# Optimization experiments

Measured on AMD Instinct MI355X. Metric: run time of the kernel, lower is better.

## Reference

```python
import jax, jax.numpy as jnp
import numpy as np

BSZ, L, D_Q, S_Q = 2, 2048, 512, 4
EPS = 1e-6


def quat_mul(a, b):
    ar, ai, aj, ak = a[..., 0], a[..., 1], a[..., 2], a[..., 3]
    br, bi, bj, bk = b[..., 0], b[..., 1], b[..., 2], b[..., 3]
    return jnp.stack((
        ar * br - ai * bi - aj * bj - ak * bk,
        ar * bi + ai * br + aj * bk - ak * bj,
        ar * bj - ai * bk + aj * br + ak * bi,
        ar * bk + ai * bj - aj * bi + ak * br,
    ), axis=-1)


def quat_inv(q):
    r, i, j, k = q[..., 0], q[..., 1], q[..., 2], q[..., 3]
    s = 1.0 / (r * r + i * i + j * j + k * k + EPS)
    return jnp.stack((r * s, -i * s, -j * s, -k * s), axis=-1)


def setup_inputs() -> dict:
    key = jax.random.key(0)
    ks = jax.random.split(key, 8)
    u = jax.random.normal(ks[0], (BSZ, L, D_Q, 4), dtype=jnp.float32)
    dt = jax.random.uniform(ks[1], (BSZ, L, D_Q), dtype=jnp.float32)
    B_in = jax.random.normal(ks[2], (BSZ, L, S_Q, 4), dtype=jnp.float32)
    C_in = jax.random.normal(ks[3], (BSZ, L, S_Q, 4), dtype=jnp.float32)
    # A_log init: log(arange(1, S_q+1)) repeated over D_q rows
    A_log = jnp.tile(jnp.log(jnp.arange(1, S_Q + 1, dtype=jnp.float32)), (D_Q, 1))
    A_i = jax.random.normal(ks[4], (D_Q, S_Q), dtype=jnp.float32) * 0.01
    A_j = jax.random.normal(ks[5], (D_Q, S_Q), dtype=jnp.float32) * 0.01
    A_k = jax.random.normal(ks[6], (D_Q, S_Q), dtype=jnp.float32) * 0.01
    return {"u": u, "dt": dt, "B_in": B_in, "C_in": C_in,
            "A_log": A_log, "A_i": A_i, "A_j": A_j, "A_k": A_k}


def reference(u, dt, B_in, C_in, A_log, A_i, A_j, A_k):
    # A quaternion: real part -exp(A_log), imaginary parts A_i/j/k  [D_q, S_q, 4]
    A_quat = jnp.stack([-jnp.exp(A_log), A_i, A_j, A_k], axis=-1)
    dt_b = dt[..., None, None]                      # [B, L, D_q, 1, 1]
    z = dt_b * A_quat                               # [B, L, D_q, S_q, 4]
    one = jnp.zeros_like(z).at[..., 0].set(1.0)     # quaternion identity
    num = one + 0.5 * z
    den = one - 0.5 * z
    den_inv = quat_inv(den)
    q = quat_mul(den_inv, num)                      # Cayley transition [B,L,D_q,S_q,4]
    dB = quat_mul(den_inv * dt_b, B_in[:, :, None])  # [B,L,D_q,S_q,4]
    Bu = quat_mul(dB, u[:, :, :, None])             # [B,L,D_q,S_q,4]

    def step(h, qb):
        qt, but = qb
        h = quat_mul(qt, h) + but
        return h, h

    h0 = jnp.zeros((u.shape[0], u.shape[2], A_quat.shape[1], 4), u.dtype)
    _, h_all = jax.lax.scan(step, h0, (jnp.swapaxes(q, 0, 1), jnp.swapaxes(Bu, 0, 1)))
    h_all = jnp.swapaxes(h_all, 0, 1)               # [B, L, D_q, S_q, 4]
    yh = quat_mul(C_in[:, :, None], h_all)
    return yh.sum(axis=3)                           # [B, L, D_q, 4]
```

## Files before the change

kernel.cpp:

```cpp
#include <hip/hip_runtime.h>

#define BSZ   2
#define LSEQ  2048
#define DQ    512
#define SQ    4
#define EPSQ  1e-6f

typedef float nfloat4 __attribute__((ext_vector_type(4)));

struct Quat { float r, i, j, k; };

__device__ __forceinline__ Quat qmul(const Quat a, const Quat b) {
    Quat o;
    o.r = a.r*b.r - a.i*b.i - a.j*b.j - a.k*b.k;
    o.i = a.r*b.i + a.i*b.r + a.j*b.k - a.k*b.j;
    o.j = a.r*b.j - a.i*b.k + a.j*b.r + a.k*b.i;
    o.k = a.r*b.k + a.i*b.j - a.j*b.i + a.k*b.r;
    return o;
}

__device__ __forceinline__ Quat qmuladd(const Quat a, const Quat b, const Quat c) {
    Quat o;
    o.r = c.r + a.r*b.r - a.i*b.i - a.j*b.j - a.k*b.k;
    o.i = c.i + a.r*b.i + a.i*b.r + a.j*b.k - a.k*b.j;
    o.j = c.j + a.r*b.j - a.i*b.k + a.j*b.r + a.k*b.i;
    o.k = c.k + a.r*b.k + a.i*b.j - a.j*b.i + a.k*b.r;
    return o;
}

__device__ __forceinline__ Quat q_of(const float4 v) { return Quat{v.x, v.y, v.z, v.w}; }
__device__ __forceinline__ float4 f4_of(const Quat q) { return make_float4(q.r, q.i, q.j, q.k); }

__device__ __forceinline__ void cayley_step(const float a, const float4 hA,
                                            const float4 Bq, const float4 uq,
                                            Quat& q, Quat& Bu) {
    const float wr = a * hA.x;
    const float wi = a * hA.y;
    const float wj = a * hA.z;
    const float wk = a * hA.w;
    const float m  = wi*wi + wj*wj + wk*wk;
    const float e  = 1.0f - wr;
    const float dd = e*e + m + EPSQ;
    const float sv = __builtin_amdgcn_rcpf(dd);
    const float s2 = sv + sv;
    q.r = sv * (1.0f - (wr*wr + m));
    q.i = s2 * wi; q.j = s2 * wj; q.k = s2 * wk;
    const Quat cd{e, wi, wj, wk};
    const Quat cb = qmul(cd, q_of(Bq));
    const float as = a * sv;
    const Quat dB{as*cb.r, as*cb.i, as*cb.j, as*cb.k};
    Bu = qmul(dB, q_of(uq));
}

__device__ __forceinline__ float4 load_hA(const float* __restrict__ Alog,
                                          const float* __restrict__ Ai,
                                          const float* __restrict__ Aj,
                                          const float* __restrict__ Ak, int idx) {
    float4 hA;
    hA.x = -0.5f * expf(Alog[idx]);
    hA.y =  0.5f * Ai[idx];
    hA.z =  0.5f * Aj[idx];
    hA.w =  0.5f * Ak[idx];
    return hA;
}

template<int NCH>
__global__ __launch_bounds__(256) void qssm_pass1(
    const float* __restrict__ u, const float* __restrict__ dt,
    const float* __restrict__ Bin,
    const float* __restrict__ Alog, const float* __restrict__ Ai,
    const float* __restrict__ Aj,   const float* __restrict__ Ak,
    float4* __restrict__ WQ, float4* __restrict__ WB)
{
    constexpr int CH = LSEQ / NCH;
    const int d = blockIdx.x * 256 + threadIdx.x;
    const int c = blockIdx.y;
    const int b = blockIdx.z;
    const int t0 = c * CH;

    float4 hA[SQ];
#pragma unroll
    for (int s = 0; s < SQ; ++s) hA[s] = load_hA(Alog, Ai, Aj, Ak, d*SQ + s);

    const float*  dtp = dt + ((size_t)(b*LSEQ + t0))*DQ + d;
    const float4* up  = (const float4*)u   + ((size_t)(b*LSEQ + t0))*DQ + d;
    const float4* Bp  = (const float4*)Bin + ((size_t)(b*LSEQ + t0))*SQ;

    Quat Q[SQ], Bc[SQ];
    {
        const float  a  = dtp[0];
        const float4 uq = up[0];
#pragma unroll
        for (int s = 0; s < SQ; ++s) {
            Quat q, Bu;
            cayley_step(a, hA[s], Bp[s], uq, q, Bu);
            Q[s] = q; Bc[s] = Bu;
        }
    }
#pragma unroll
    for (int j = 1; j < CH; ++j) {
        const float  a  = dtp[(size_t)j*DQ];
        const float4 uq = up[(size_t)j*DQ];
#pragma unroll
        for (int s = 0; s < SQ; ++s) {
            Quat q, Bu;
            cayley_step(a, hA[s], Bp[j*SQ + s], uq, q, Bu);
            Bc[s] = qmuladd(q, Bc[s], Bu);
            Q[s]  = qmul(q, Q[s]);
        }
    }
#pragma unroll
    for (int s = 0; s < SQ; ++s) {
        const size_t idx = ((size_t)(b*SQ + s)*NCH + c)*DQ + d;
        WQ[idx] = f4_of(Q[s]);
        WB[idx] = f4_of(Bc[s]);
    }
}

template<int NCH>
__global__ __launch_bounds__(256) void qssm_pass2(
    const float4* __restrict__ WQ, float4* __restrict__ WB)
{
    constexpr int GS = 16;
    constexpr int NG = NCH / GS;
    __shared__ float4 QL[NG][16];
    __shared__ float4 BL[NG][16];
    __shared__ float4 HS[NG][16];

    const int t  = threadIdx.x;
    const int i  = t & 15;
    const int g  = t >> 4;
    const int bs = blockIdx.x >> 5;
    const int d  = (blockIdx.x & 31) * 16 + i;
    const size_t chbase = (size_t)bs * NCH * DQ + d;

    size_t idx = chbase + (size_t)(g * GS) * DQ;
    Quat Qa = q_of(WQ[idx]);
    Quat Ba = q_of(WB[idx]);
#pragma unroll
    for (int j = 1; j < GS; ++j) {
        idx += DQ;
        const Quat Qc = q_of(WQ[idx]);
        const Quat Bc = q_of(WB[idx]);
        Ba = qmuladd(Qc, Ba, Bc);
        Qa = qmul(Qc, Qa);
    }
    QL[g][i] = f4_of(Qa);
    BL[g][i] = f4_of(Ba);
    __syncthreads();

    if (t < 16) {
        Quat h{0.f, 0.f, 0.f, 0.f};
#pragma unroll
        for (int gg = 0; gg < NG; ++gg) {
            HS[gg][t] = f4_of(h);
            h = qmuladd(q_of(QL[gg][t]), h, q_of(BL[gg][t]));
        }
    }
    __syncthreads();

    Quat h = q_of(HS[g][i]);
    idx = chbase + (size_t)(g * GS) * DQ;
#pragma unroll
    for (int j = 0; j < GS; ++j) {
        const Quat Qc = q_of(WQ[idx]);
        const Quat Bc = q_of(WB[idx]);
        WB[idx] = f4_of(h);
        h = qmuladd(Qc, h, Bc);
        idx += DQ;
    }
}

template<int NCH>
__global__ __launch_bounds__(256) void qssm_pass3(
    const float* __restrict__ u, const float* __restrict__ dt,
    const float* __restrict__ Bin, const float* __restrict__ Cin,
    const float* __restrict__ Alog, const float* __restrict__ Ai,
    const float* __restrict__ Aj,   const float* __restrict__ Ak,
    const float4* __restrict__ WB, float* __restrict__ out)
{
    constexpr int CH = LSEQ / NCH;
    const int d = blockIdx.x * 256 + threadIdx.x;
    const int c = blockIdx.y;
    const int b = blockIdx.z;
    const int t0 = c * CH;

    float4 hA[SQ];
    Quat   h[SQ];
#pragma unroll
    for (int s = 0; s < SQ; ++s) {
        hA[s] = load_hA(Alog, Ai, Aj, Ak, d*SQ + s);
        h[s] = q_of(WB[((size_t)(b*SQ + s)*NCH + c)*DQ + d]);
    }
    const float*  dtp  = dt + ((size_t)(b*LSEQ + t0))*DQ + d;
    const float4* up   = (const float4*)u   + ((size_t)(b*LSEQ + t0))*DQ + d;
    const float4* Bp   = (const float4*)Bin + ((size_t)(b*LSEQ + t0))*SQ;
    const float4* Cp   = (const float4*)Cin + ((size_t)(b*LSEQ + t0))*SQ;
    nfloat4*      outp = (nfloat4*)out + ((size_t)(b*LSEQ + t0))*DQ + d;

#pragma unroll
    for (int j = 0; j < CH; ++j) {
        const float  a  = dtp[(size_t)j*DQ];
        const float4 uq = up[(size_t)j*DQ];
        Quat y{0.f, 0.f, 0.f, 0.f};
#pragma unroll
        for (int s = 0; s < SQ; ++s) {
            const float4 Cq = Cp[j*SQ + s];
            Quat q, Bu;
            cayley_step(a, hA[s], Bp[j*SQ + s], uq, q, Bu);
            h[s] = qmuladd(q, h[s], Bu);
            y = qmuladd(q_of(Cq), h[s], y);
        }
        const nfloat4 yv = {y.r, y.i, y.j, y.k};
        __builtin_nontemporal_store(yv, &outp[(size_t)j*DQ]);
    }
}

template<int NCH>
static void launch_all(const float* u, const float* dt, const float* Bin,
                       const float* Cin, const float* Alog, const float* Ai,
                       const float* Aj, const float* Ak,
                       float* out, void* d_ws, hipStream_t stream) {
    const size_t elems = (size_t)BSZ * SQ * NCH * DQ;
    float4* WQ = (float4*)d_ws;
    float4* WB = WQ + elems;
    dim3 g(DQ / 256, NCH, BSZ);
    qssm_pass1<NCH><<<g, 256, 0, stream>>>(u, dt, Bin, Alog, Ai, Aj, Ak, WQ, WB);
    qssm_pass2<NCH><<<(BSZ*SQ*DQ)/16, 16*(NCH/16), 0, stream>>>(WQ, WB);
    qssm_pass3<NCH><<<g, 256, 0, stream>>>(u, dt, Bin, Cin, Alog, Ai, Aj, Ak, WB, out);
}

extern "C" void kernel_launch(void* const* d_in, const int* in_sizes, int n_in,
                              void* d_out, int out_size, void* d_ws, size_t ws_size,
                              hipStream_t stream) {
    const float* u    = (const float*)d_in[0];
    const float* dt   = (const float*)d_in[1];
    const float* Bin  = (const float*)d_in[2];
    const float* Cin  = (const float*)d_in[3];
    const float* Alog = (const float*)d_in[4];
    const float* Ai   = (const float*)d_in[5];
    const float* Aj   = (const float*)d_in[6];
    const float* Ak   = (const float*)d_in[7];
    float* out = (float*)d_out;

    auto ws_need = [](int nch) -> size_t {
        return 2ull * BSZ * SQ * (size_t)nch * DQ * sizeof(float4);
    };
    if (ws_size >= ws_need(256)) {
        launch_all<256>(u, dt, Bin, Cin, Alog, Ai, Aj, Ak, out, d_ws, stream);
    } else if (ws_size >= ws_need(128)) {
        launch_all<128>(u, dt, Bin, Cin, Alog, Ai, Aj, Ak, out, d_ws, stream);
    } else {
        launch_all<64>(u, dt, Bin, Cin, Alog, Ai, Aj, Ak, out, d_ws, stream);
    }
}
```

Measured before the change: 164.8 us.

## Split state dimension across threads in scan passes to raise parallelism

Pass 1 now launches twice as many blocks, each thread handling two of the four state quaternions instead of all four. Pass 3 assigns the two state halves to the upper and lower 32 lanes of each wavefront and combines the partial outputs with a cross-lane shuffle before the store. Loop unrolling drops from full to 2 and pointer increments replace indexed addressing, with __expf replacing expf. This is meant to cut per-thread register pressure and add occupancy and parallelism, at the cost of loading u and dt redundantly per state half and the extra shuffle work.

```diff
diff --git a/kernel.cpp b/kernel.cpp
--- a/kernel.cpp
+++ b/kernel.cpp
@@ -57,7 +57,7 @@
                                           const float* __restrict__ Aj,
                                           const float* __restrict__ Ak, int idx) {
     float4 hA;
-    hA.x = -0.5f * expf(Alog[idx]);
+    hA.x = -0.5f * __expf(Alog[idx]);
     hA.y =  0.5f * Ai[idx];
     hA.z =  0.5f * Aj[idx];
     hA.w =  0.5f * Ak[idx];
@@ -73,47 +73,51 @@
     float4* __restrict__ WQ, float4* __restrict__ WB)
 {
     constexpr int CH = LSEQ / NCH;
-    const int d = blockIdx.x * 256 + threadIdx.x;
-    const int c = blockIdx.y;
-    const int b = blockIdx.z;
+    const int d  = blockIdx.x * 256 + threadIdx.x;
+    const int c  = blockIdx.y;
+    const int b  = blockIdx.z >> 1;
+    const int s0 = (blockIdx.z & 1) * 2;
     const int t0 = c * CH;
 
-    float4 hA[SQ];
-#pragma unroll
-    for (int s = 0; s < SQ; ++s) hA[s] = load_hA(Alog, Ai, Aj, Ak, d*SQ + s);
-
-    const float*  dtp = dt + ((size_t)(b*LSEQ + t0))*DQ + d;
-    const float4* up  = (const float4*)u   + ((size_t)(b*LSEQ + t0))*DQ + d;
-    const float4* Bp  = (const float4*)Bin + ((size_t)(b*LSEQ + t0))*SQ;
-
-    Quat Q[SQ], Bc[SQ];
+    float4 hA[2];
+    hA[0] = load_hA(Alog, Ai, Aj, Ak, d*SQ + s0);
+    hA[1] = load_hA(Alog, Ai, Aj, Ak, d*SQ + s0 + 1);
+
+    const int base = (b*LSEQ + t0);
+    const float*  dtp = dt + (size_t)base*DQ + d;
+    const float4* up  = (const float4*)u   + (size_t)base*DQ + d;
+    const float4* Bp  = (const float4*)Bin + (size_t)base*SQ + s0;
+
+    Quat Q[2], Bc[2];
     {
-        const float  a  = dtp[0];
-        const float4 uq = up[0];
-#pragma unroll
-        for (int s = 0; s < SQ; ++s) {
+        const float  a  = *dtp;
+        const float4 uq = *up;
+#pragma unroll
+        for (int ss = 0; ss < 2; ++ss) {
             Quat q, Bu;
-            cayley_step(a, hA[s], Bp[s], uq, q, Bu);
-            Q[s] = q; Bc[s] = Bu;
-        }
-    }
-#pragma unroll
+            cayley_step(a, hA[ss], Bp[ss], uq, q, Bu);
+            Q[ss] = q; Bc[ss] = Bu;
+        }
+        dtp += DQ; up += DQ; Bp += SQ;
+    }
+#pragma unroll 2
     for (int j = 1; j < CH; ++j) {
-        const float  a  = dtp[(size_t)j*DQ];
-        const float4 uq = up[(size_t)j*DQ];
-#pragma unroll
-        for (int s = 0; s < SQ; ++s) {
+        const float  a  = *dtp;
+        const float4 uq = *up;
+#pragma unroll
+        for (int ss = 0; ss < 2; ++ss) {
             Quat q, Bu;
-            cayley_step(a, hA[s], Bp[j*SQ + s], uq, q, Bu);
-            Bc[s] = qmuladd(q, Bc[s], Bu);
-            Q[s]  = qmul(q, Q[s]);
-        }
-    }
-#pragma unroll
-    for (int s = 0; s < SQ; ++s) {
-        const size_t idx = ((size_t)(b*SQ + s)*NCH + c)*DQ + d;
-        WQ[idx] = f4_of(Q[s]);
-        WB[idx] = f4_of(Bc[s]);
+            cayley_step(a, hA[ss], Bp[ss], uq, q, Bu);
+            Bc[ss] = qmuladd(q, Bc[ss], Bu);
+            Q[ss]  = qmul(q, Q[ss]);
+        }
+        dtp += DQ; up += DQ; Bp += SQ;
+    }
+#pragma unroll
+    for (int ss = 0; ss < 2; ++ss) {
+        const size_t idx = ((size_t)(b*SQ + s0 + ss)*NCH + c)*DQ + d;
+        WQ[idx] = f4_of(Q[ss]);
+        WB[idx] = f4_of(Bc[ss]);
     }
 }
 
@@ -180,39 +184,53 @@
     const float4* __restrict__ WB, float* __restrict__ out)
 {
     constexpr int CH = LSEQ / NCH;
-    const int d = blockIdx.x * 256 + threadIdx.x;
+    const int t    = threadIdx.x;
+    const int lane = t & 63;
+    const int wv   = t >> 6;
+    const int dl   = lane & 31;
+    const int sh   = lane >> 5;
+    const int s0   = sh * 2;
+    const int d = blockIdx.x * 128 + wv * 32 + dl;
     const int c = blockIdx.y;
     const int b = blockIdx.z;
     const int t0 = c * CH;
 
-    float4 hA[SQ];
-    Quat   h[SQ];
-#pragma unroll
-    for (int s = 0; s < SQ; ++s) {
-        hA[s] = load_hA(Alog, Ai, Aj, Ak, d*SQ + s);
-        h[s] = q_of(WB[((size_t)(b*SQ + s)*NCH + c)*DQ + d]);
-    }
-    const float*  dtp  = dt + ((size_t)(b*LSEQ + t0))*DQ + d;
-    const float4* up   = (const float4*)u   + ((size_t)(b*LSEQ + t0))*DQ + d;
-    const float4* Bp   = (const float4*)Bin + ((size_t)(b*LSEQ + t0))*SQ;
-    const float4* Cp   = (const float4*)Cin + ((size_t)(b*LSEQ + t0))*SQ;
-    nfloat4*      outp = (nfloat4*)out + ((size_t)(b*LSEQ + t0))*DQ + d;
-
-#pragma unroll
+    float4 hA[2];
+    Quat   h[2];
+#pragma unroll
+    for (int ss = 0; ss < 2; ++ss) {
+        hA[ss] = load_hA(Alog, Ai, Aj, Ak, d*SQ + s0 + ss);
+        h[ss] = q_of(WB[((size_t)(b*SQ + s0 + ss)*NCH + c)*DQ + d]);
+    }
+    const int base = (b*LSEQ + t0);
+    const float*  dtp  = dt + (size_t)base*DQ + d;
+    const float4* up   = (const float4*)u   + (size_t)base*DQ + d;
+    const float4* Bp   = (const float4*)Bin + (size_t)base*SQ + s0;
+    const float4* Cp   = (const float4*)Cin + (size_t)base*SQ + s0;
+    nfloat4*      outp = (nfloat4*)out + (size_t)base*DQ + d;
+
+#pragma unroll 2
     for (int j = 0; j < CH; ++j) {
-        const float  a  = dtp[(size_t)j*DQ];
-        const float4 uq = up[(size_t)j*DQ];
+        const float  a  = *dtp;
+        const float4 uq = *up;
         Quat y{0.f, 0.f, 0.f, 0.f};
 #pragma unroll
-        for (int s = 0; s < SQ; ++s) {
-            const float4 Cq = Cp[j*SQ + s];
+        for (int ss = 0; ss < 2; ++ss) {
+            const float4 Cq = Cp[ss];
             Quat q, Bu;
-            cayley_step(a, hA[s], Bp[j*SQ + s], uq, q, Bu);
-            h[s] = qmuladd(q, h[s], Bu);
-            y = qmuladd(q_of(Cq), h[s], y);
-        }
-        const nfloat4 yv = {y.r, y.i, y.j, y.k};
-        __builtin_nontemporal_store(yv, &outp[(size_t)j*DQ]);
+            cayley_step(a, hA[ss], Bp[ss], uq, q, Bu);
+            h[ss] = qmuladd(q, h[ss], Bu);
+            y = qmuladd(q_of(Cq), h[ss], y);
+        }
+        y.r += __shfl_xor(y.r, 32);
+        y.i += __shfl_xor(y.i, 32);
+        y.j += __shfl_xor(y.j, 32);
+        y.k += __shfl_xor(y.k, 32);
+        if (sh == 0) {
+            const nfloat4 yv = {y.r, y.i, y.j, y.k};
+            __builtin_nontemporal_store(yv, outp);
+        }
+        dtp += DQ; up += DQ; Bp += SQ; Cp += SQ; outp += DQ;
     }
 }
 
@@ -224,10 +242,11 @@
     const size_t elems = (size_t)BSZ * SQ * NCH * DQ;
     float4* WQ = (float4*)d_ws;
     float4* WB = WQ + elems;
-    dim3 g(DQ / 256, NCH, BSZ);
-    qssm_pass1<NCH><<<g, 256, 0, stream>>>(u, dt, Bin, Alog, Ai, Aj, Ak, WQ, WB);
+    dim3 g1(DQ / 256, NCH, BSZ * 2);
+    qssm_pass1<NCH><<<g1, 256, 0, stream>>>(u, dt, Bin, Alog, Ai, Aj, Ak, WQ, WB);
     qssm_pass2<NCH><<<(BSZ*SQ*DQ)/16, 16*(NCH/16), 0, stream>>>(WQ, WB);
-    qssm_pass3<NCH><<<g, 256, 0, stream>>>(u, dt, Bin, Cin, Alog, Ai, Aj, Ak, WB, out);
+    dim3 g3(DQ / 128, NCH, BSZ);
+    qssm_pass3<NCH><<<g3, 256, 0, stream>>>(u, dt, Bin, Cin, Alog, Ai, Aj, Ak, WB, out);
 }
 
 extern "C" void kernel_launch(void* const* d_in, const int* in_sizes, int n_in,
```

Result: faster. 161.2 us (-2.2%).
